# Performance work log

Hardware: AMD Instinct MI355X
Metric: run time of the kernel (lower is better)

## Reference

```python
import jax, jax.numpy as jnp
from jax import lax
import numpy as np

B, CIN, COUT, H, W, K = 32, 128, 256, 64, 64, 3


def _conv_L(x, w, b):
    # pointwise (1x1) conv: x (B,C,H,W), w (Cin,Cout), b (Cout,)
    return jnp.einsum('bchw,co->bohw', x, w) + b[None, :, None, None]


def _dw_along_W(x, w, b):
    # per-channel depthwise 1D correlation along W, VALID padding
    C = x.shape[1]
    y = lax.conv_general_dilated(x, w[:, None, None, :], (1, 1), 'VALID',
                                 dimension_numbers=('NCHW', 'OIHW', 'NCHW'),
                                 feature_group_count=C)
    return y + b[None, :, None, None]


def _dw_along_H(x, w, b):
    # per-channel depthwise 1D correlation along H, VALID padding
    C = x.shape[1]
    y = lax.conv_general_dilated(x, w[:, None, :, None], (1, 1), 'VALID',
                                 dimension_numbers=('NCHW', 'OIHW', 'NCHW'),
                                 feature_group_count=C)
    return y + b[None, :, None, None]


def setup_inputs() -> dict:
    key = jax.random.key(0)
    ks = jax.random.split(key, 13)
    u = lambda kk, shape: jax.random.uniform(kk, shape, jnp.float32, -0.1, 0.1)
    return {
        'x': jax.random.normal(ks[0], (B, CIN, H, W), jnp.float32),
        'L1_w': u(ks[1], (CIN, COUT)), 'L1_b': u(ks[2], (COUT,)),
        'V1_w': u(ks[3], (COUT, K)),   'V1_b': u(ks[4], (COUT,)),
        'H1_w': u(ks[5], (COUT, K)),   'H1_b': u(ks[6], (COUT,)),
        'L2_w': u(ks[7], (COUT, COUT)), 'L2_b': u(ks[8], (COUT,)),
        'V2_w': u(ks[9], (COUT, K)),   'V2_b': u(ks[10], (COUT,)),
        'H2_w': u(ks[11], (COUT, K)),  'H2_b': u(ks[12], (COUT,)),
    }


def reference(x, L1_w, L1_b, V1_w, V1_b, H1_w, H1_b,
              L2_w, L2_b, V2_w, V2_b, H2_w, H2_b):
    p = K // 2
    y = _conv_L(x, L1_w, L1_b)            # (B,COUT,H,W)
    y = _dw_along_H(y, V1_w, V1_b)        # (B,COUT,H-K+1,W)
    y = _dw_along_W(y, H1_w, H1_b)        # (B,COUT,H-K+1,W-K+1)
    y = _conv_L(y, L2_w, L2_b)
    y = jnp.pad(y, ((0, 0), (0, 0), (p, p), (p, p)))  # back to (B,COUT,H,W)
    y = _dw_along_H(y, V2_w, V2_b)
    y = _dw_along_W(y, H2_w, H2_b)        # (B,COUT,H-K+1,W-K+1)
    return y
```

## Files before the change

kernel.cpp:

```cpp
#include <hip/hip_runtime.h>
#include <stdint.h>

#define BB  32
#define CIN 128
#define CO  256
#define HH  64
#define WW  64
#define HW  4096
#define OH  62
#define OW  62
#define OHW 3844

typedef __attribute__((ext_vector_type(8))) short  short8;
typedef __attribute__((ext_vector_type(4))) float  f32x4;
typedef __attribute__((ext_vector_type(4))) ushort ushort4v;

__device__ __forceinline__ ushort f2bf(float f) {
  uint32_t u = __builtin_bit_cast(uint32_t, f);
  u += 0x7FFFu + ((u >> 16) & 1u);
  return (ushort)(u >> 16);
}
__device__ __forceinline__ float bf2f(ushort h) {
  uint32_t u = ((uint32_t)h) << 16;
  return __builtin_bit_cast(float, u);
}

__global__ void k_wt(const float* __restrict__ w, ushort* __restrict__ wt,
                     int kdim, int ndim) {
  int e = blockIdx.x * 256 + threadIdx.x;
  if (e >= kdim * ndim) return;
  int co = e / kdim, ci = e - co * kdim;
  wt[e] = f2bf(w[(size_t)ci * ndim + co]);
}

template<bool GATHER>
__global__ __launch_bounds__(512) void k_gemm(
    const void* __restrict__ src, const ushort* __restrict__ wt,
    const float* __restrict__ bias, ushort* __restrict__ out,
    int hw_total, int ktot)
{
  __shared__ union {
    struct { ushort Wq[256][40]; ushort Xq[64][40]; } s;
    ushort Rp[64][260];
  } U;
  __shared__ float biasS[256];

  const int t    = threadIdx.x;
  const int b    = blockIdx.y;
  const int hw0  = blockIdx.x * 64;
  const int wid  = t >> 6;
  const int lane = t & 63;
  const int wn   = wid & 3;
  const int wm   = wid >> 2;
  const int l15  = lane & 15;
  const int l4   = lane >> 4;

  if (t < 256) biasS[t] = bias[t];

  f32x4 acc[4][2];
  #pragma unroll
  for (int i = 0; i < 4; ++i)
    #pragma unroll
    for (int j = 0; j < 2; ++j)
      #pragma unroll
      for (int k = 0; k < 4; ++k) acc[i][j][k] = 0.f;

  const int ksteps = ktot >> 5;
  for (int ks = 0; ks < ksteps; ++ks) {
    const int ci0 = ks * 32;
    __syncthreads();

    #pragma unroll
    for (int it = 0; it < 2; ++it) {
      int c  = it * 512 + t;
      int co = c >> 2, seg = c & 3;
      const ushort* p = wt + (size_t)co * ktot + ci0 + seg * 8;
      short8 v = *(const short8*)p;
      *(short8*)&U.s.Wq[co][seg * 8] = v;
    }
    if (t < 256) {
      if (GATHER) {
        int hw = t & 63, g = t >> 6;
        const float* xp = (const float*)src
            + (size_t)b * CIN * HW + (size_t)(ci0 + g * 8) * HW + hw0 + hw;
        short8 v;
        #pragma unroll
        for (int i = 0; i < 8; ++i) v[i] = (short)f2bf(xp[(size_t)i * HW]);
        *(short8*)&U.s.Xq[hw][g * 8] = v;
      } else {
        int hw = t >> 2, seg = t & 3;
        short8 v;
        if (hw0 + hw < hw_total) {
          const ushort* p = (const ushort*)src
              + (size_t)b * hw_total * ktot + (size_t)(hw0 + hw) * ktot + ci0 + seg * 8;
          v = *(const short8*)p;
        } else {
          #pragma unroll
          for (int i = 0; i < 8; ++i) v[i] = 0;
        }
        *(short8*)&U.s.Xq[hw][seg * 8] = v;
      }
    }
    __syncthreads();

    short8 af[4], bx[2];
    #pragma unroll
    for (int i = 0; i < 4; ++i)
      af[i] = *(const short8*)&U.s.Wq[wn * 64 + i * 16 + l15][l4 * 8];
    #pragma unroll
    for (int j = 0; j < 2; ++j)
      bx[j] = *(const short8*)&U.s.Xq[wm * 32 + j * 16 + l15][l4 * 8];
    #pragma unroll
    for (int i = 0; i < 4; ++i)
      #pragma unroll
      for (int j = 0; j < 2; ++j)
        acc[i][j] = __builtin_amdgcn_mfma_f32_16x16x32_bf16(af[i], bx[j], acc[i][j], 0, 0, 0);
  }

  __syncthreads();

  #pragma unroll
  for (int i = 0; i < 4; ++i) {
    int co_b = wn * 64 + i * 16 + l4 * 4;
    #pragma unroll
    for (int j = 0; j < 2; ++j) {
      int hw_ = wm * 32 + j * 16 + l15;
      ushort4v v;
      #pragma unroll
      for (int k = 0; k < 4; ++k)
        v[k] = f2bf(acc[i][j][k] + biasS[co_b + k]);
      *(ushort4v*)&U.Rp[hw_][co_b] = v;
    }
  }
  __syncthreads();

  const size_t ob = (size_t)b * hw_total * CO;
  #pragma unroll
  for (int it = 0; it < 8; ++it) {
    int row = it * 8 + (t >> 6);
    int seg = t & 63;
    if (hw0 + row < hw_total) {
      ushort4v v = *(const ushort4v*)&U.Rp[row][seg * 4];
      *(ushort4v*)(out + ob + (size_t)(hw0 + row) * CO + seg * 4) = v;
    }
  }
}

__global__ __launch_bounds__(256) void k_dw1(
    const ushort* __restrict__ y1t, const float* __restrict__ vw,
    const float* __restrict__ vb, const float* __restrict__ hwt,
    const float* __restrict__ hb, ushort* __restrict__ t1t)
{
  const int c = threadIdx.x, h = blockIdx.x, b = blockIdx.y;
  const float v0 = vw[c * 3 + 0], v1 = vw[c * 3 + 1], v2 = vw[c * 3 + 2];
  const float h0 = hwt[c * 3 + 0], h1 = hwt[c * 3 + 1], h2 = hwt[c * 3 + 2];
  const float cst = vb[c] * (h0 + h1 + h2) + hb[c];
  const ushort* base = y1t + (size_t)b * HW * CO + c;
  ushort* ob = t1t + ((size_t)b * OHW + (size_t)h * OW) * CO + c;

  auto vcol = [&](int s) -> float {
    return v0 * bf2f(base[(size_t)((h + 0) * WW + s) * CO])
         + v1 * bf2f(base[(size_t)((h + 1) * WW + s) * CO])
         + v2 * bf2f(base[(size_t)((h + 2) * WW + s) * CO]);
  };
  float c0 = vcol(0), c1 = vcol(1);
  for (int w = 0; w < OW; ++w) {
    float c2 = vcol(w + 2);
    ob[(size_t)w * CO] = f2bf(h0 * c0 + h1 * c1 + h2 * c2 + cst);
    c0 = c1; c1 = c2;
  }
}

__global__ __launch_bounds__(256) void k_dw2(
    const ushort* __restrict__ t2t, const float* __restrict__ vw,
    const float* __restrict__ vb, const float* __restrict__ hwt,
    const float* __restrict__ hb, float* __restrict__ outp)
{
  __shared__ float S[256][17];
  const int c = threadIdx.x, h = blockIdx.x, b = blockIdx.y;
  const float v0 = vw[c * 3 + 0], v1 = vw[c * 3 + 1], v2 = vw[c * 3 + 2];
  const float h0 = hwt[c * 3 + 0], h1 = hwt[c * 3 + 1], h2 = hwt[c * 3 + 2];
  const float cst = vb[c] * (h0 + h1 + h2) + hb[c];
  const ushort* base = t2t + (size_t)b * OHW * CO + c;
  const bool rm = (h - 1 >= 0), rp = (h + 1 < OH);

  auto vcol = [&](int s) -> float {
    float a = v1 * bf2f(base[(size_t)(h * OW + s) * CO]);
    if (rm) a += v0 * bf2f(base[(size_t)((h - 1) * OW + s) * CO]);
    if (rp) a += v2 * bf2f(base[(size_t)((h + 1) * OW + s) * CO]);
    return a;
  };

  float c0 = 0.f;
  float c1 = vcol(0);
  float* outb = outp + (size_t)b * CO * OHW + (size_t)h * OW;

  for (int chunk = 0; chunk < 4; ++chunk) {
    int w0 = chunk * 16;
    #pragma unroll
    for (int jj = 0; jj < 16; ++jj) {
      int w = w0 + jj;
      if (w < OW) {
        float c2 = (w + 1 < OW) ? vcol(w + 1) : 0.f;
        S[c][jj] = h0 * c0 + h1 * c1 + h2 * c2 + cst;
        c0 = c1; c1 = c2;
      }
    }
    __syncthreads();
    int wloc = c & 15, cg = c >> 4;
    #pragma unroll
    for (int k = 0; k < 16; ++k) {
      int cc = k * 16 + cg;
      if (w0 + wloc < OW)
        outb[(size_t)cc * OHW + w0 + wloc] = S[cc][wloc];
    }
    __syncthreads();
  }
}

extern "C" void kernel_launch(void* const* d_in, const int* in_sizes, int n_in,
                              void* d_out, int out_size, void* d_ws, size_t ws_size,
                              hipStream_t stream) {
  const float* x   = (const float*)d_in[0];
  const float* L1w = (const float*)d_in[1];
  const float* L1b = (const float*)d_in[2];
  const float* V1w = (const float*)d_in[3];
  const float* V1b = (const float*)d_in[4];
  const float* H1w = (const float*)d_in[5];
  const float* H1b = (const float*)d_in[6];
  const float* L2w = (const float*)d_in[7];
  const float* L2b = (const float*)d_in[8];
  const float* V2w = (const float*)d_in[9];
  const float* V2b = (const float*)d_in[10];
  const float* H2w = (const float*)d_in[11];
  const float* H2b = (const float*)d_in[12];

  char* ws = (char*)d_ws;
  ushort* y1t = (ushort*)ws;
  ushort* w1t = (ushort*)(ws + (size_t)67108864);
  ushort* w2t = (ushort*)(ws + (size_t)67108864 + 65536);
  ushort* t2t = (ushort*)ws;
  ushort* t1t = (ushort*)d_out;

  k_wt<<<dim3((CIN * CO + 255) / 256), dim3(256), 0, stream>>>(L1w, w1t, CIN, CO);
  k_wt<<<dim3((CO * CO + 255) / 256), dim3(256), 0, stream>>>(L2w, w2t, CO, CO);

  k_gemm<true><<<dim3(HW / 64, BB), dim3(512), 0, stream>>>(
      (const void*)x, w1t, L1b, y1t, HW, CIN);

  k_dw1<<<dim3(OH, BB), dim3(256), 0, stream>>>(y1t, V1w, V1b, H1w, H1b, t1t);

  k_gemm<false><<<dim3((OHW + 63) / 64, BB), dim3(512), 0, stream>>>(
      (const void*)t1t, w2t, L2b, t2t, OHW, CO);

  k_dw2<<<dim3(OH, BB), dim3(256), 0, stream>>>(t2t, V2w, V2b, H2w, H2b, (float*)d_out);
}
```

Measured before the change: 375.8 us.

## Switch intermediates to channel-planar NCHW layout with LDS-tiled depthwise kernels

```diff
diff --git a/kernel.cpp b/kernel.cpp
--- a/kernel.cpp
+++ b/kernel.cpp
@@ -14,6 +14,7 @@
 typedef __attribute__((ext_vector_type(8))) short  short8;
 typedef __attribute__((ext_vector_type(4))) float  f32x4;
 typedef __attribute__((ext_vector_type(4))) ushort ushort4v;
+typedef __attribute__((ext_vector_type(2))) ushort ushort2v;
 
 __device__ __forceinline__ ushort f2bf(float f) {
   uint32_t u = __builtin_bit_cast(uint32_t, f);
@@ -39,9 +40,9 @@
     const float* __restrict__ bias, ushort* __restrict__ out,
     int hw_total, int ktot)
 {
-  __shared__ union {
+  __shared__ union alignas(16) {
     struct { ushort Wq[256][40]; ushort Xq[64][40]; } s;
-    ushort Rp[64][260];
+    ushort Cp[256][72];
   } U;
   __shared__ float biasS[256];
 
@@ -79,27 +80,25 @@
       *(short8*)&U.s.Wq[co][seg * 8] = v;
     }
     if (t < 256) {
+      int hw = t & 63, g = t >> 6;
+      short8 v;
       if (GATHER) {
-        int hw = t & 63, g = t >> 6;
         const float* xp = (const float*)src
             + (size_t)b * CIN * HW + (size_t)(ci0 + g * 8) * HW + hw0 + hw;
-        short8 v;
         #pragma unroll
         for (int i = 0; i < 8; ++i) v[i] = (short)f2bf(xp[(size_t)i * HW]);
-        *(short8*)&U.s.Xq[hw][g * 8] = v;
       } else {
-        int hw = t >> 2, seg = t & 3;
-        short8 v;
         if (hw0 + hw < hw_total) {
-          const ushort* p = (const ushort*)src
-              + (size_t)b * hw_total * ktot + (size_t)(hw0 + hw) * ktot + ci0 + seg * 8;
-          v = *(const short8*)p;
+          const ushort* xp = (const ushort*)src
+              + ((size_t)b * CO + (ci0 + g * 8)) * hw_total + hw0 + hw;
+          #pragma unroll
+          for (int i = 0; i < 8; ++i) v[i] = (short)xp[(size_t)i * hw_total];
         } else {
           #pragma unroll
           for (int i = 0; i < 8; ++i) v[i] = 0;
         }
-        *(short8*)&U.s.Xq[hw][seg * 8] = v;
       }
+      *(short8*)&U.s.Xq[hw][g * 8] = v;
     }
     __syncthreads();
 
@@ -121,100 +120,113 @@
 
   #pragma unroll
   for (int i = 0; i < 4; ++i) {
-    int co_b = wn * 64 + i * 16 + l4 * 4;
     #pragma unroll
     for (int j = 0; j < 2; ++j) {
-      int hw_ = wm * 32 + j * 16 + l15;
-      ushort4v v;
+      int hwl = wm * 32 + j * 16 + l15;
       #pragma unroll
-      for (int k = 0; k < 4; ++k)
-        v[k] = f2bf(acc[i][j][k] + biasS[co_b + k]);
-      *(ushort4v*)&U.Rp[hw_][co_b] = v;
-    }
-  }
-  __syncthreads();
-
-  const size_t ob = (size_t)b * hw_total * CO;
-  #pragma unroll
-  for (int it = 0; it < 8; ++it) {
-    int row = it * 8 + (t >> 6);
-    int seg = t & 63;
-    if (hw0 + row < hw_total) {
-      ushort4v v = *(const ushort4v*)&U.Rp[row][seg * 4];
-      *(ushort4v*)(out + ob + (size_t)(hw0 + row) * CO + seg * 4) = v;
+      for (int k = 0; k < 4; ++k) {
+        int co = wn * 64 + i * 16 + l4 * 4 + k;
+        U.Cp[co][hwl] = f2bf(acc[i][j][k] + biasS[co]);
+      }
+    }
+  }
+  __syncthreads();
+
+  const size_t ob = (size_t)b * CO * (size_t)hw_total + hw0;
+  if (hw0 + 64 <= hw_total) {
+    #pragma unroll
+    for (int p = 0; p < 4; ++p) {
+      int co = p * 64 + (t >> 3), ch = t & 7;
+      ushort4v lo = *(const ushort4v*)&U.Cp[co][ch * 8];
+      ushort4v hi = *(const ushort4v*)&U.Cp[co][ch * 8 + 4];
+      ushort* q = out + ob + (size_t)co * hw_total + ch * 8;
+      *(ushort4v*)q = lo;
+      *(ushort4v*)(q + 4) = hi;
+    }
+  } else {
+    int rem = hw_total - hw0;
+    #pragma unroll
+    for (int p = 0; p < 2; ++p) {
+      int co = p * 128 + (t >> 2);
+      for (int w = (t & 3); w < rem; w += 4)
+        out[ob + (size_t)co * hw_total + w] = U.Cp[co][w];
     }
   }
 }
 
 __global__ __launch_bounds__(256) void k_dw1(
-    const ushort* __restrict__ y1t, const float* __restrict__ vw,
+    const ushort* __restrict__ y1, const float* __restrict__ vw,
     const float* __restrict__ vb, const float* __restrict__ hwt,
-    const float* __restrict__ hb, ushort* __restrict__ t1t)
+    const float* __restrict__ hb, ushort* __restrict__ t1)
 {
-  const int c = threadIdx.x, h = blockIdx.x, b = blockIdx.y;
+  __shared__ ushort P[64][66];
+  const int t = threadIdx.x, c = blockIdx.x, b = blockIdx.y;
+  const ushort* src = y1 + ((size_t)b * CO + c) * HW;
+  #pragma unroll
+  for (int k = 0; k < 8; ++k) {
+    int e2 = t + k * 256;
+    int h = e2 >> 5, w = (e2 & 31) * 2;
+    *(ushort2v*)&P[h][w] = *(const ushort2v*)(src + h * WW + w);
+  }
   const float v0 = vw[c * 3 + 0], v1 = vw[c * 3 + 1], v2 = vw[c * 3 + 2];
   const float h0 = hwt[c * 3 + 0], h1 = hwt[c * 3 + 1], h2 = hwt[c * 3 + 2];
   const float cst = vb[c] * (h0 + h1 + h2) + hb[c];
-  const ushort* base = y1t + (size_t)b * HW * CO + c;
-  ushort* ob = t1t + ((size_t)b * OHW + (size_t)h * OW) * CO + c;
-
-  auto vcol = [&](int s) -> float {
-    return v0 * bf2f(base[(size_t)((h + 0) * WW + s) * CO])
-         + v1 * bf2f(base[(size_t)((h + 1) * WW + s) * CO])
-         + v2 * bf2f(base[(size_t)((h + 2) * WW + s) * CO]);
-  };
-  float c0 = vcol(0), c1 = vcol(1);
-  for (int w = 0; w < OW; ++w) {
-    float c2 = vcol(w + 2);
-    ob[(size_t)w * CO] = f2bf(h0 * c0 + h1 * c1 + h2 * c2 + cst);
-    c0 = c1; c1 = c2;
+  __syncthreads();
+  if (t < 248) {
+    const int h = t >> 2, seg = t & 3;
+    const int w0 = seg * 16, n = (seg == 3) ? 14 : 16;
+    auto vcol = [&](int s) -> float {
+      return v0 * bf2f(P[h][s]) + v1 * bf2f(P[h + 1][s]) + v2 * bf2f(P[h + 2][s]);
+    };
+    float c0 = vcol(w0), c1 = vcol(w0 + 1);
+    ushort* ob = t1 + ((size_t)b * CO + c) * OHW + h * OW + w0;
+    for (int j = 0; j < n; ++j) {
+      float c2 = vcol(w0 + j + 2);
+      ob[j] = f2bf(h0 * c0 + h1 * c1 + h2 * c2 + cst);
+      c0 = c1; c1 = c2;
+    }
   }
 }
 
 __global__ __launch_bounds__(256) void k_dw2(
-    const ushort* __restrict__ t2t, const float* __restrict__ vw,
+    const ushort* __restrict__ t2, const float* __restrict__ vw,
     const float* __restrict__ vb, const float* __restrict__ hwt,
     const float* __restrict__ hb, float* __restrict__ outp)
 {
-  __shared__ float S[256][17];
-  const int c = threadIdx.x, h = blockIdx.x, b = blockIdx.y;
+  __shared__ ushort P[62][66];
+  const int t = threadIdx.x, c = blockIdx.x, b = blockIdx.y;
+  const ushort* src = t2 + ((size_t)b * CO + c) * OHW;
+  #pragma unroll
+  for (int k = 0; k < 8; ++k) {
+    int e2 = t + k * 256;
+    if (e2 < 1922) {
+      int e = e2 * 2;
+      int h = e / 62, w = e - h * 62;
+      *(ushort2v*)&P[h][w] = *(const ushort2v*)(src + e);
+    }
+  }
   const float v0 = vw[c * 3 + 0], v1 = vw[c * 3 + 1], v2 = vw[c * 3 + 2];
   const float h0 = hwt[c * 3 + 0], h1 = hwt[c * 3 + 1], h2 = hwt[c * 3 + 2];
   const float cst = vb[c] * (h0 + h1 + h2) + hb[c];
-  const ushort* base = t2t + (size_t)b * OHW * CO + c;
-  const bool rm = (h - 1 >= 0), rp = (h + 1 < OH);
-
-  auto vcol = [&](int s) -> float {
-    float a = v1 * bf2f(base[(size_t)(h * OW + s) * CO]);
-    if (rm) a += v0 * bf2f(base[(size_t)((h - 1) * OW + s) * CO]);
-    if (rp) a += v2 * bf2f(base[(size_t)((h + 1) * OW + s) * CO]);
-    return a;
-  };
-
-  float c0 = 0.f;
-  float c1 = vcol(0);
-  float* outb = outp + (size_t)b * CO * OHW + (size_t)h * OW;
-
-  for (int chunk = 0; chunk < 4; ++chunk) {
-    int w0 = chunk * 16;
-    #pragma unroll
-    for (int jj = 0; jj < 16; ++jj) {
-      int w = w0 + jj;
-      if (w < OW) {
-        float c2 = (w + 1 < OW) ? vcol(w + 1) : 0.f;
-        S[c][jj] = h0 * c0 + h1 * c1 + h2 * c2 + cst;
-        c0 = c1; c1 = c2;
-      }
-    }
-    __syncthreads();
-    int wloc = c & 15, cg = c >> 4;
-    #pragma unroll
-    for (int k = 0; k < 16; ++k) {
-      int cc = k * 16 + cg;
-      if (w0 + wloc < OW)
-        outb[(size_t)cc * OHW + w0 + wloc] = S[cc][wloc];
-    }
-    __syncthreads();
+  __syncthreads();
+  if (t < 248) {
+    const int h = t >> 2, seg = t & 3;
+    const int w0 = seg * 16, n = (seg == 3) ? 14 : 16;
+    const bool rm = (h > 0), rp = (h < OH - 1);
+    auto vcol = [&](int s) -> float {
+      if ((unsigned)s >= (unsigned)OW) return 0.f;
+      float a = v1 * bf2f(P[h][s]);
+      if (rm) a += v0 * bf2f(P[h - 1][s]);
+      if (rp) a += v2 * bf2f(P[h + 1][s]);
+      return a;
+    };
+    float c0 = vcol(w0 - 1), c1 = vcol(w0);
+    float* ob = outp + ((size_t)b * CO + c) * OHW + h * OW + w0;
+    for (int j = 0; j < n; ++j) {
+      float c2 = vcol(w0 + j + 1);
+      ob[j] = h0 * c0 + h1 * c1 + h2 * c2 + cst;
+      c0 = c1; c1 = c2;
+    }
   }
 }
 
@@ -236,22 +248,22 @@
   const float* H2b = (const float*)d_in[12];
 
   char* ws = (char*)d_ws;
-  ushort* y1t = (ushort*)ws;
+  ushort* y1n = (ushort*)ws;
   ushort* w1t = (ushort*)(ws + (size_t)67108864);
   ushort* w2t = (ushort*)(ws + (size_t)67108864 + 65536);
-  ushort* t2t = (ushort*)ws;
-  ushort* t1t = (ushort*)d_out;
+  ushort* t2n = (ushort*)ws;
+  ushort* t1n = (ushort*)d_out;
 
   k_wt<<<dim3((CIN * CO + 255) / 256), dim3(256), 0, stream>>>(L1w, w1t, CIN, CO);
   k_wt<<<dim3((CO * CO + 255) / 256), dim3(256), 0, stream>>>(L2w, w2t, CO, CO);
 
   k_gemm<true><<<dim3(HW / 64, BB), dim3(512), 0, stream>>>(
-      (const void*)x, w1t, L1b, y1t, HW, CIN);
-
-  k_dw1<<<dim3(OH, BB), dim3(256), 0, stream>>>(y1t, V1w, V1b, H1w, H1b, t1t);
+      (const void*)x, w1t, L1b, y1n, HW, CIN);
+
+  k_dw1<<<dim3(CO, BB), dim3(256), 0, stream>>>(y1n, V1w, V1b, H1w, H1b, t1n);
 
   k_gemm<false><<<dim3((OHW + 63) / 64, BB), dim3(512), 0, stream>>>(
-      (const void*)t1t, w2t, L2b, t2t, OHW, CO);
-
-  k_dw2<<<dim3(OH, BB), dim3(256), 0, stream>>>(t2t, V2w, V2b, H2w, H2b, (float*)d_out);
-}
+      (const void*)t1n, w2t, L2b, t2n, OHW, CO);
+
+  k_dw2<<<dim3(CO, BB), dim3(256), 0, stream>>>(t2n, V2w, V2b, H2w, H2b, (float*)d_out);
+}
```

Result: slower. 434.5 us (+15.6%).
